# Optimization experiments

Hardware: AMD Instinct MI355X
Metric: run time of the kernel (lower is better)

The kernel has to match this reference:

```python
import jax, jax.numpy as jnp
import numpy as np
import math

B, S, T = 32, 128, 64
FEAT = 16
H = 1024
V = 32000


def _gru_step(x, h, wih, whh, bih, bhh):
    # torch nn.GRU cell: gates ordered (r, z, n)
    gi = x @ wih.T + bih
    gh = h @ whh.T + bhh
    ir, iz, in_ = jnp.split(gi, 3, axis=-1)
    hr, hz, hn = jnp.split(gh, 3, axis=-1)
    r = jax.nn.sigmoid(ir + hr)
    z = jax.nn.sigmoid(iz + hz)
    n = jnp.tanh(in_ + r * hn)
    return (1.0 - z) * n + z * h


def _forward(features, target_tokens, temp_W, temp_b, hum_W, hum_b, cloud_W, cloud_b,
             time_W, time_b, other_W, other_b, fi_W, fi_b,
             enc_wih, enc_whh, enc_bih, enc_bhh, emb, attn_W, attn_b,
             dec_wih, dec_whh, dec_bih, dec_bhh, out_W, out_b):
    b = features.shape[0]
    # per-feature projections (dropout = identity in eval mode)
    temp = features[:, :, 0:1] @ temp_W.T + temp_b
    hum = features[:, :, 1:2] @ hum_W.T + hum_b
    cloud = features[:, :, 2:3] @ cloud_W.T + cloud_b
    time = features[:, :, -5:-3] @ time_W.T + time_b
    other_in = jnp.concatenate([features[:, :, 3:-5], features[:, :, -3:]], axis=2)
    other = other_in @ other_W.T + other_b
    concat = jnp.concatenate([temp, hum, cloud, time, other], axis=2)  # [B,S,2H]
    proj = jnp.tanh(concat @ fi_W.T + fi_b)  # [B,S,H]

    # encoder GRU over time
    def enc_step(h, x):
        h2 = _gru_step(x, h, enc_wih, enc_whh, enc_bih, enc_bhh)
        return h2, h2
    h0 = jnp.zeros((b, H), proj.dtype)
    h_last, enc_outs = jax.lax.scan(enc_step, h0, proj.transpose(1, 0, 2))
    enc_out = enc_outs.transpose(1, 0, 2)  # [B,S,H]

    # attention keys computed once (loop-invariant in the original)
    keys = enc_out @ attn_W.T + attn_b  # [B,S,H]
    scale = 1.0 / math.sqrt(H)

    # decoder: teacher_forcing_ratio = 1.0 -> input at step t is target_tokens[:, t-1]
    def dec_step(h, tok):
        e = emb[tok]  # [B,H]
        scores = jnp.einsum('bh,bsh->bs', h, keys) * scale
        w = jax.nn.softmax(scores, axis=-1)
        ctx = jnp.einsum('bs,bsh->bh', w, enc_out)
        x = jnp.concatenate([e, ctx], axis=-1)  # [B,2H]
        h2 = _gru_step(x, h, dec_wih, dec_whh, dec_bih, dec_bhh)
        pred = jnp.concatenate([h2, ctx], axis=-1) @ out_W.T + out_b  # [B,V]
        return h2, pred

    _, preds = jax.lax.scan(dec_step, h_last, target_tokens[:, :-1].T)  # [T-1,B,V]
    outputs = jnp.zeros((b, target_tokens.shape[1], V), preds.dtype)
    outputs = outputs.at[:, 0, target_tokens[0, 0]].set(1.0)
    outputs = outputs.at[:, 1:, :].set(preds.transpose(1, 0, 2))
    return outputs


def setup_inputs() -> dict:
    key = jax.random.key(0)
    ks = jax.random.split(key, 32)
    nrm = lambda k, sh: jax.random.normal(k, sh, jnp.float32) * 0.05
    Hq = H // 4
    d = {}
    d['features'] = jax.random.normal(ks[0], (B, S, FEAT), jnp.float32)
    d['target_tokens'] = jax.random.randint(ks[1], (B, T), 0, V, dtype=jnp.int32)
    d['temp_W'] = nrm(ks[2], (Hq, 1)); d['temp_b'] = nrm(ks[3], (Hq,))
    d['hum_W'] = nrm(ks[4], (Hq, 1)); d['hum_b'] = nrm(ks[5], (Hq,))
    d['cloud_W'] = nrm(ks[6], (Hq, 1)); d['cloud_b'] = nrm(ks[7], (Hq,))
    d['time_W'] = nrm(ks[8], (Hq, 2)); d['time_b'] = nrm(ks[9], (Hq,))
    d['other_W'] = nrm(ks[10], (H, FEAT - 5)); d['other_b'] = nrm(ks[11], (H,))
    d['fi_W'] = nrm(ks[12], (H, 2 * H)); d['fi_b'] = nrm(ks[13], (H,))
    d['enc_wih'] = nrm(ks[14], (3 * H, H)); d['enc_whh'] = nrm(ks[15], (3 * H, H))
    d['enc_bih'] = nrm(ks[16], (3 * H,)); d['enc_bhh'] = nrm(ks[17], (3 * H,))
    d['emb'] = nrm(ks[18], (V, H))
    d['attn_W'] = nrm(ks[19], (H, H)); d['attn_b'] = nrm(ks[20], (H,))
    d['dec_wih'] = nrm(ks[21], (3 * H, 2 * H)); d['dec_whh'] = nrm(ks[22], (3 * H, H))
    d['dec_bih'] = nrm(ks[23], (3 * H,)); d['dec_bhh'] = nrm(ks[24], (3 * H,))
    d['out_W'] = nrm(ks[25], (V, 2 * H)); d['out_b'] = nrm(ks[26], (V,))
    return d


def reference(features, target_tokens, temp_W, temp_b, hum_W, hum_b, cloud_W, cloud_b,
              time_W, time_b, other_W, other_b, fi_W, fi_b,
              enc_wih, enc_whh, enc_bih, enc_bhh, emb, attn_W, attn_b,
              dec_wih, dec_whh, dec_bih, dec_bhh, out_W, out_b):
    return _forward(features, target_tokens, temp_W, temp_b, hum_W, hum_b, cloud_W, cloud_b,
                    time_W, time_b, other_W, other_b, fi_W, fi_b,
                    enc_wih, enc_whh, enc_bih, enc_bhh, emb, attn_W, attn_b,
                    dec_wih, dec_whh, dec_bih, dec_bhh, out_W, out_b)
```

## Files before the change

### kernel.cpp

```cpp
#include <hip/hip_runtime.h>

typedef float f32x4 __attribute__((ext_vector_type(4)));
typedef __bf16 bf16x8 __attribute__((ext_vector_type(8)));

#define DI static __device__ __forceinline__

DI unsigned short f2bf(float f) {
  unsigned u = __float_as_uint(f);
  u = (u + 0x7fffu + ((u >> 16) & 1u)) >> 16;
  return (unsigned short)u;
}
DI unsigned pk2(float lo, float hi) {
  return (unsigned)f2bf(lo) | ((unsigned)f2bf(hi) << 16);
}
DI float bflo(unsigned u) { return __uint_as_float(u << 16); }
DI float bfhi(unsigned u) { return __uint_as_float(u & 0xffff0000u); }
DI float sigm(float x) { return 1.0f / (1.0f + expf(-x)); }

DI void gl_lds16(const unsigned short* g, unsigned short* l) {
  __builtin_amdgcn_global_load_lds(
      (const __attribute__((address_space(1))) unsigned int*)g,
      (__attribute__((address_space(3))) unsigned int*)l, 16, 0, 0);
}

DI void st32_sc1(unsigned* p, unsigned v) {
  __hip_atomic_store(p, v, __ATOMIC_RELAXED, __HIP_MEMORY_SCOPE_AGENT);
}
DI void st64_sc1(unsigned long long* p, unsigned long long v) {
  __hip_atomic_store(p, v, __ATOMIC_RELAXED, __HIP_MEMORY_SCOPE_AGENT);
}
DI int ldw(const int* p) {
  return __hip_atomic_load(p, __ATOMIC_RELAXED, __HIP_MEMORY_SCOPE_AGENT);
}
DI void stw(int* p, int v) {
  __hip_atomic_store(p, v, __ATOMIC_RELAXED, __HIP_MEMORY_SCOPE_AGENT);
}

DI void waitrel(const int* relbase, int repl, int target) {
  const int* w = relbase + repl * 32;
  for (;;) {
    int v = 0;
    if ((threadIdx.x & 63) == 0) v = ldw(w);
    v = __shfl(v, 0);
    if (v >= target) break;
    __builtin_amdgcn_s_sleep(2);
  }
  asm volatile("" ::: "memory");
}
DI void strel(int* relbase, int v) {
  int l = threadIdx.x & 63;
  if (l < 8) stw(relbase + l * 32, v);
}

__global__ void k_fold(const float* __restrict__ tW, const float* __restrict__ tb,
                       const float* __restrict__ hW, const float* __restrict__ hb,
                       const float* __restrict__ cW, const float* __restrict__ cb,
                       const float* __restrict__ tiW, const float* __restrict__ tib,
                       const float* __restrict__ oW, const float* __restrict__ ob,
                       const float* __restrict__ fiW, const float* __restrict__ fib,
                       float* __restrict__ M, float* __restrict__ b0v)
{
  int g = blockIdx.x * 256 + threadIdx.x;
  if (g >= 1024 * 17) return;
  int h = g / 17, f = g - h * 17;
  const float* fw = fiW + (size_t)h * 2048;
  float s = 0.f;
  if (f == 16) {
    for (int k = 0; k < 256; ++k) s += fw[k] * tb[k];
    for (int k = 0; k < 256; ++k) s += fw[256 + k] * hb[k];
    for (int k = 0; k < 256; ++k) s += fw[512 + k] * cb[k];
    for (int k = 0; k < 256; ++k) s += fw[768 + k] * tib[k];
    for (int r = 0; r < 1024; ++r) s += fw[1024 + r] * ob[r];
    b0v[h] = s + fib[h];
  } else if (f == 0) {
    for (int k = 0; k < 256; ++k) s += fw[k] * tW[k];
    M[h * 16 + 0] = s;
  } else if (f == 1) {
    for (int k = 0; k < 256; ++k) s += fw[256 + k] * hW[k];
    M[h * 16 + 1] = s;
  } else if (f == 2) {
    for (int k = 0; k < 256; ++k) s += fw[512 + k] * cW[k];
    M[h * 16 + 2] = s;
  } else if (f == 11) {
    for (int k = 0; k < 256; ++k) s += fw[768 + k] * tiW[2 * k];
    M[h * 16 + 11] = s;
  } else if (f == 12) {
    for (int k = 0; k < 256; ++k) s += fw[768 + k] * tiW[2 * k + 1];
    M[h * 16 + 12] = s;
  } else {
    int col = (f <= 10) ? (f - 3) : (f - 5);
    for (int r = 0; r < 1024; ++r) s += fw[1024 + r] * oW[r * 11 + col];
    M[h * 16 + f] = s;
  }
}

__global__ __launch_bounds__(256)
void k_proj(const float* __restrict__ feat, const float* __restrict__ M,
            const float* __restrict__ b0v, unsigned short* __restrict__ proj)
{
  __shared__ float ft[16];
  int bs = blockIdx.x;
  int h = blockIdx.y * 256 + threadIdx.x;
  if (threadIdx.x < 16) ft[threadIdx.x] = feat[bs * 16 + threadIdx.x];
  __syncthreads();
  float sum = b0v[h];
  const float* mr = M + h * 16;
#pragma unroll
  for (int f = 0; f < 16; ++f) sum += mr[f] * ft[f];
  proj[(size_t)bs * 1024 + h] = f2bf(tanhf(sum));
}

__global__ void k_conv(const float* __restrict__ s, unsigned short* __restrict__ d, int n8)
{
  for (long i = (long)blockIdx.x * 256 + threadIdx.x; i < n8; i += (long)gridDim.x * 256) {
    const float* p = s + i * 8;
    f32x4 a = *(const f32x4*)p, b = *(const f32x4*)(p + 4);
    uint4 o;
    o.x = pk2(a[0], a[1]); o.y = pk2(a[2], a[3]);
    o.z = pk2(b[0], b[1]); o.w = pk2(b[2], b[3]);
    *(uint4*)(d + i * 8) = o;
  }
}

__global__ void k_conv_str(const float* __restrict__ s, unsigned short* __restrict__ d)
{
  int r = blockIdx.x;
  int c = threadIdx.x * 4;
  f32x4 a = *(const f32x4*)(s + (size_t)r * 2048 + c);
  uint2 o; o.x = pk2(a[0], a[1]); o.y = pk2(a[2], a[3]);
  *(uint2*)(d + (size_t)r * 1024 + c) = o;
}

__global__ void k_gather_e(const int* __restrict__ toks, const float* __restrict__ emb,
                           unsigned short* __restrict__ e_bf)
{
  int row = blockIdx.x;
  int t = row >> 5, b = row & 31;
  unsigned short* dst = e_bf + (size_t)row * 1024 + threadIdx.x * 4;
  if (t < 63) {
    int tok = toks[b * 64 + t];
    f32x4 a = *(const f32x4*)(emb + (size_t)tok * 1024 + threadIdx.x * 4);
    uint2 o; o.x = pk2(a[0], a[1]); o.y = pk2(a[2], a[3]);
    *(uint2*)dst = o;
  } else {
    uint2 o; o.x = 0u; o.y = 0u;
    *(uint2*)dst = o;
  }
}

__global__ void k_onehot(const int* __restrict__ toks, float* __restrict__ out)
{
  int i = blockIdx.x * 256 + threadIdx.x;
  if (i >= 32 * 32000) return;
  int b = i / 32000, v = i - b * 32000;
  out[(size_t)b * 64 * 32000 + v] = (v == toks[0]) ? 1.0f : 0.0f;
}

template<int MODE>
__global__ __launch_bounds__(256)
void gemm_bf(const unsigned short* __restrict__ A, const unsigned short* __restrict__ B,
             const float* __restrict__ bias, float* __restrict__ Cf,
             unsigned short* __restrict__ Cb,
             int tiles_m, int K, int lda, int ldb, int ldc, int coloff)
{
  __shared__ unsigned short As[4096];
  __shared__ unsigned short Bs[4096];
  const int nblk = gridDim.x;
  const int cpx = nblk >> 3;
  const int bid = blockIdx.x;
  const int id = (bid & 7) * cpx + (bid >> 3);
  const int tm = id % tiles_m, tn = id / tiles_m;
  const int tid = threadIdx.x;
  const int lane = tid & 63, wave = tid >> 6;
  const int wm = (wave & 1) << 6, wn = (wave >> 1) << 6;
  const int r0 = tid >> 2, kc0 = (tid & 3) << 3;
  const unsigned short* ga0 = A + (size_t)(tm * 128 + r0) * lda + kc0;
  const unsigned short* ga1 = A + (size_t)(tm * 128 + 64 + r0) * lda + kc0;
  const unsigned short* gb0 = B + (size_t)(tn * 128 + r0) * ldb + kc0;
  const unsigned short* gb1 = B + (size_t)(tn * 128 + 64 + r0) * ldb + kc0;
  const int lr = lane & 15, lkb = (lane >> 4) << 3;

  f32x4 acc[4][4];
#pragma unroll
  for (int m = 0; m < 4; ++m)
#pragma unroll
    for (int n = 0; n < 4; ++n) { acc[m][n][0]=0.f; acc[m][n][1]=0.f; acc[m][n][2]=0.f; acc[m][n][3]=0.f; }

  for (int kt = 0; kt < K; kt += 32) {
    __syncthreads();
    gl_lds16(ga0 + kt, &As[tid * 8]);
    gl_lds16(ga1 + kt, &As[(tid + 256) * 8]);
    gl_lds16(gb0 + kt, &Bs[tid * 8]);
    gl_lds16(gb1 + kt, &Bs[(tid + 256) * 8]);
    __syncthreads();
    bf16x8 af[4], bfv[4];
#pragma unroll
    for (int m = 0; m < 4; ++m) af[m] = *(const bf16x8*)&As[(wm + m * 16 + lr) * 32 + lkb];
#pragma unroll
    for (int n = 0; n < 4; ++n) bfv[n] = *(const bf16x8*)&Bs[(wn + n * 16 + lr) * 32 + lkb];
#pragma unroll
    for (int m = 0; m < 4; ++m)
#pragma unroll
      for (int n = 0; n < 4; ++n)
        acc[m][n] = __builtin_amdgcn_mfma_f32_16x16x32_bf16(af[m], bfv[n], acc[m][n], 0, 0, 0);
  }

#pragma unroll
  for (int m = 0; m < 4; ++m) {
    int rb = tm * 128 + wm + m * 16 + ((lane >> 4) << 2);
#pragma unroll
    for (int n = 0; n < 4; ++n) {
      int c = tn * 128 + wn + n * 16 + lr;
      float bb = bias[c];
#pragma unroll
      for (int i = 0; i < 4; ++i) {
        float v = acc[m][n][i] + bb;
        int r = rb + i;
        if (MODE == 0) {
          Cf[(size_t)r * ldc + c] = v;
        } else if (MODE == 1) {
          Cb[(size_t)r * ldc + c] = f2bf(v);
        } else {
          if (r < 2016) {
            int t = r >> 5, b2 = r & 31;
            Cf[((size_t)b2 * 64 + t + 1) * 32000 + coloff + c] = v;
          }
        }
      }
    }
  }
}

__global__ __launch_bounds__(256, 1)
void k_enc_scan(const float* __restrict__ gi_all, const float* __restrict__ whh,
                const float* __restrict__ bhh, float* __restrict__ hfp,
                unsigned short* __restrict__ enc_bf,
                int* __restrict__ arrE, int* __restrict__ relE)
{
  const int tid = threadIdx.x;
  const int blk = blockIdx.x;
  if (blk == 64) {
    if (tid < 64) {
      for (int g = 1; g <= 128; ++g) {
        for (;;) {
          int v = ldw(&arrE[tid << 4]);
          if (__all(v >= g)) break;
          __builtin_amdgcn_s_sleep(1);
        }
        asm volatile("" ::: "memory");
        strel(relE, g);
      }
    }
    return;
  }

  __shared__ unsigned short W[48 * 1024];
  __shared__ float Cred[4 * 2 * 3 * 64 * 4];
  const int lane = tid & 63, wave = tid >> 6;
  const int j0 = blk * 16;
  const int repl = blk & 7;

  for (int i = tid; i < 48 * 128; i += 256) {
    int r = i >> 7, c = i & 127;
    int gr = ((r >> 4) << 10) + j0 + (r & 15);
    const float* src = whh + ((size_t)gr << 10) + (c << 3);
    f32x4 a = *(const f32x4*)src, b = *(const f32x4*)(src + 4);
    uint4 o;
    o.x = pk2(a[0], a[1]); o.y = pk2(a[2], a[3]);
    o.z = pk2(b[0], b[1]); o.w = pk2(b[2], b[3]);
    *(uint4*)&W[(r << 10) + ((c ^ (r & 7)) << 3)] = o;
  }
  __syncthreads();

  int cb[2], cj[2], clb[2], creg[2], cm[2];
  float bh0[2], bh1[2], bh2[2];
  float hp[2] = {0.f, 0.f};
#pragma unroll
  for (int cc = 0; cc < 2; ++cc) {
    int cell = tid + (cc << 8);
    cb[cc] = cell >> 4; cj[cc] = cell & 15;
    clb[cc] = ((cb[cc] & 15) >> 2) * 16;
    creg[cc] = cb[cc] & 3; cm[cc] = cb[cc] >> 4;
    bh0[cc] = bhh[j0 + cj[cc]];
    bh1[cc] = bhh[1024 + j0 + cj[cc]];
    bh2[cc] = bhh[2048 + j0 + cj[cc]];
  }

#pragma unroll 1
  for (int s = 0; s < 128; ++s) {
    float gp[2][3];
#pragma unroll
    for (int cc = 0; cc < 2; ++cc) {
      const float* gi = gi_all + ((size_t)cb[cc] * 128 + s) * 3072 + j0 + cj[cc];
      gp[cc][0] = gi[0]; gp[cc][1] = gi[1024]; gp[cc][2] = gi[2048];
    }

    f32x4 acc[2][3];
#pragma unroll
    for (int m = 0; m < 2; ++m)
#pragma unroll
      for (int n = 0; n < 3; ++n) { acc[m][n][0]=0.f; acc[m][n][1]=0.f; acc[m][n][2]=0.f; acc[m][n][3]=0.f; }

    if (s > 0) {
      waitrel(relE, repl, s);
      const unsigned short* hr = enc_bf + (size_t)(s - 1) * 1024;
      const int k0 = wave << 8;
      bf16x8 af[2][8];
#pragma unroll
      for (int kk = 0; kk < 8; ++kk) {
        int k = k0 + kk * 32 + ((lane >> 4) << 3);
        af[0][kk] = *(const bf16x8*)(hr + (size_t)(lane & 15) * 131072 + k);
        af[1][kk] = *(const bf16x8*)(hr + (size_t)(16 + (lane & 15)) * 131072 + k);
      }
#pragma unroll
      for (int kk = 0; kk < 8; ++kk) {
        int c = ((k0 + kk * 32) >> 3) + (lane >> 4);
#pragma unroll
        for (int n = 0; n < 3; ++n) {
          int wr = n * 16 + (lane & 15);
          bf16x8 bfr = *(const bf16x8*)&W[(wr << 10) + ((c ^ (wr & 7)) << 3)];
          acc[0][n] = __builtin_amdgcn_mfma_f32_16x16x32_bf16(af[0][kk], bfr, acc[0][n], 0, 0, 0);
          acc[1][n] = __builtin_amdgcn_mfma_f32_16x16x32_bf16(af[1][kk], bfr, acc[1][n], 0, 0, 0);
        }
      }
    }
#pragma unroll
    for (int m = 0; m < 2; ++m)
#pragma unroll
      for (int n = 0; n < 3; ++n)
        *(f32x4*)&Cred[((((wave * 2 + m) * 3 + n) * 64) + lane) << 2] = acc[m][n];
    __syncthreads();

    float h2v[2];
#pragma unroll
    for (int cc = 0; cc < 2; ++cc) {
      int lj = clb[cc] + cj[cc], reg = creg[cc], m = cm[cc];
      float Cr = 0.f, Cz = 0.f, Cn = 0.f;
#pragma unroll
      for (int w = 0; w < 4; ++w) {
        Cr += Cred[((((w * 2 + m) * 3 + 0) * 64 + lj) << 2) + reg];
        Cz += Cred[((((w * 2 + m) * 3 + 1) * 64 + lj) << 2) + reg];
        Cn += Cred[((((w * 2 + m) * 3 + 2) * 64 + lj) << 2) + reg];
      }
      float r = sigm(gp[cc][0] + Cr + bh0[cc]);
      float z = sigm(gp[cc][1] + Cz + bh1[cc]);
      float n = tanhf(gp[cc][2] + r * (Cn + bh2[cc]));
      float h2 = (1.f - z) * n + z * hp[cc];
      h2v[cc] = h2; hp[cc] = h2;
    }
    if (s == 127) {
      hfp[cb[0] * 1024 + j0 + cj[0]] = h2v[0];
      hfp[cb[1] * 1024 + j0 + cj[1]] = h2v[1];
    }
    unsigned short s0 = f2bf(h2v[0]), s1 = f2bf(h2v[1]);
    unsigned o0 = (unsigned)__shfl_xor((int)(unsigned)s0, 1);
    unsigned o1 = (unsigned)__shfl_xor((int)(unsigned)s1, 1);
    if ((tid & 1) == 0) {
      int j = cj[0];
      st32_sc1((unsigned*)&enc_bf[((size_t)cb[0] * 128 + s) * 1024 + j0 + j],
               (unsigned)s0 | (o0 << 16));
      st32_sc1((unsigned*)&enc_bf[((size_t)cb[1] * 128 + s) * 1024 + j0 + j],
               (unsigned)s1 | (o1 << 16));
    }
    __syncthreads();
    if (tid == 0) stw(&arrE[blk << 4], s + 1);
  }
}

__global__ __launch_bounds__(256, 1)
void k_dec_scan(const float* __restrict__ gi_e, const float* __restrict__ whh,
                const float* __restrict__ wih, const float* __restrict__ bhh,
                const unsigned short* __restrict__ keys,
                const unsigned short* __restrict__ enc_bf,
                unsigned short* __restrict__ hcat, const float* __restrict__ hfp0,
                int* __restrict__ arrC, int* __restrict__ arrH,
                int* __restrict__ relD)
{
  const int tid = threadIdx.x;
  const int blk = blockIdx.x;
  const int repl = blk & 7;

  if (blk == 160) {
    if (tid < 64) {
      for (int t = 0; t < 63; ++t) {
        for (;;) {
          int v = (tid < 32) ? ldw(&arrC[tid << 4]) : 0x7fffffff;
          if (__all(v >= t + 1)) break;
          __builtin_amdgcn_s_sleep(1);
        }
        asm volatile("" ::: "memory");
        strel(relD, 2 * t + 1);
        for (;;) {
          int v0 = ldw(&arrH[(tid * 2) << 4]);
          int v1 = ldw(&arrH[(tid * 2 + 1) << 4]);
          if (__all(v0 >= t + 1 && v1 >= t + 1)) break;
          __builtin_amdgcn_s_sleep(1);
        }
        asm volatile("" ::: "memory");
        strel(relD, 2 * t + 2);
      }
    }
    return;
  }

  if (blk < 32) {
    __shared__ unsigned short hsh[1024];
    __shared__ float sarr[128];
    __shared__ float earr[128];
    const int b = blk;
#pragma unroll 1
    for (int t = 0; t < 63; ++t) {
      if (t) waitrel(relD, repl, 2 * t);
      const unsigned short* hsrc = (t == 0)
          ? (enc_bf + (size_t)b * 131072 + (size_t)127 * 1024)
          : (hcat + ((size_t)(t - 1) * 32 + b) * 2048);
      *(uint2*)&hsh[tid * 4] = *(const uint2*)(hsrc + tid * 4);
      __syncthreads();
      {
        int sp = tid >> 1, kh = (tid & 1) << 9;
        const unsigned short* kr = keys + ((size_t)b * 128 + sp) * 1024 + kh;
        float a0 = 0.f, a1 = 0.f, a2 = 0.f, a3 = 0.f;
#pragma unroll 8
        for (int c = 0; c < 512; c += 8) {
          uint4 kv = *(const uint4*)(kr + c);
          uint4 hv = *(const uint4*)&hsh[kh + c];
          a0 += bflo(kv.x) * bflo(hv.x) + bfhi(kv.x) * bfhi(hv.x);
          a1 += bflo(kv.y) * bflo(hv.y) + bfhi(kv.y) * bfhi(hv.y);
          a2 += bflo(kv.z) * bflo(hv.z) + bfhi(kv.z) * bfhi(hv.z);
          a3 += bflo(kv.w) * bflo(hv.w) + bfhi(kv.w) * bfhi(hv.w);
        }
        float a = (a0 + a1) + (a2 + a3);
        a += __shfl_xor(a, 1);
        if ((tid & 1) == 0) sarr[sp] = a * 0.03125f;
      }
      __syncthreads();
      float m0 = -1e30f, m1 = -1e30f, m2 = -1e30f, m3 = -1e30f;
#pragma unroll 8
      for (int i2 = 0; i2 < 128; i2 += 4) {
        m0 = fmaxf(m0, sarr[i2]); m1 = fmaxf(m1, sarr[i2 + 1]);
        m2 = fmaxf(m2, sarr[i2 + 2]); m3 = fmaxf(m3, sarr[i2 + 3]);
      }
      float mx = fmaxf(fmaxf(m0, m1), fmaxf(m2, m3));
      if (tid < 128) earr[tid] = expf(sarr[tid] - mx);
      __syncthreads();
      float s0 = 0.f, s1 = 0.f, s2 = 0.f, s3 = 0.f;
#pragma unroll 8
      for (int i2 = 0; i2 < 128; i2 += 4) {
        s0 += earr[i2]; s1 += earr[i2 + 1]; s2 += earr[i2 + 2]; s3 += earr[i2 + 3];
      }
      float winv = 1.f / ((s0 + s1) + (s2 + s3));
      f32x4 cacc; cacc[0]=0.f; cacc[1]=0.f; cacc[2]=0.f; cacc[3]=0.f;
      const unsigned short* eb = enc_bf + ((size_t)b << 17) + tid * 4;
#pragma unroll 4
      for (int s2i = 0; s2i < 128; ++s2i) {
        float w = earr[s2i] * winv;
        uint2 ev = *(const uint2*)(eb + ((size_t)s2i << 10));
        cacc[0] += w * bflo(ev.x); cacc[1] += w * bfhi(ev.x);
        cacc[2] += w * bflo(ev.y); cacc[3] += w * bfhi(ev.y);
      }
      unsigned long long cw = (unsigned long long)pk2(cacc[0], cacc[1])
                            | ((unsigned long long)pk2(cacc[2], cacc[3]) << 32);
      st64_sc1((unsigned long long*)(hcat + ((size_t)t * 32 + b) * 2048 + 1024 + tid * 4), cw);
      __syncthreads();
      if (tid == 0) stw(&arrC[blk << 4], t + 1);
    }
    return;
  }

  __shared__ unsigned short Wh[32 * 1024];
  __shared__ unsigned short Wx[32 * 1024];
  __shared__ float Cred[4 * 2 * 2 * 64 * 4];
  const int lane = tid & 63, wave = tid >> 6;
  const int gblk = blk - 32;
  const int j0 = gblk * 8;

  for (int i = tid; i < 32 * 128; i += 256) {
    int r = i >> 7, c = i & 127;
    int off = (r << 10) + ((c ^ (r & 7)) << 3);
    uint4 oh, ox;
    oh.x = oh.y = oh.z = oh.w = 0u; ox = oh;
    if (r < 24) {
      int gr = ((r >> 3) << 10) + j0 + (r & 7);
      const float* sh = whh + ((size_t)gr << 10) + (c << 3);
      f32x4 a = *(const f32x4*)sh, b = *(const f32x4*)(sh + 4);
      oh.x = pk2(a[0], a[1]); oh.y = pk2(a[2], a[3]);
      oh.z = pk2(b[0], b[1]); oh.w = pk2(b[2], b[3]);
      const float* sx = wih + ((size_t)gr << 11) + 1024 + (c << 3);
      f32x4 e = *(const f32x4*)sx, f = *(const f32x4*)(sx + 4);
      ox.x = pk2(e[0], e[1]); ox.y = pk2(e[2], e[3]);
      ox.z = pk2(f[0], f[1]); ox.w = pk2(f[2], f[3]);
    }
    *(uint4*)&Wh[off] = oh;
    *(uint4*)&Wx[off] = ox;
  }
  __syncthreads();

  const int gb = tid >> 3, gj = tid & 7;
  const int glb = ((gb & 15) >> 2) * 16;
  const int greg = gb & 3, gm = gb >> 4;
  const float bh0 = bhh[j0 + gj];
  const float bh1 = bhh[1024 + j0 + gj];
  const float bh2 = bhh[2048 + j0 + gj];
  float hpv = hfp0[gb * 1024 + j0 + gj];

#pragma unroll 1
  for (int t = 0; t < 63; ++t) {
    const float* gie = gi_e + ((size_t)t * 32 + gb) * 3072 + j0 + gj;
    float g0 = gie[0], g1 = gie[1024], g2 = gie[2048];

    const int part = wave >> 1;
    const int kh2 = (wave & 1) << 9;
    const unsigned short* abase;
    size_t astr;
    const unsigned short* Wl;
    if (part == 0) {
      if (t) waitrel(relD, repl, 2 * t);
      if (t == 0) { abase = enc_bf + (size_t)127 * 1024; astr = 131072; }
      else { abase = hcat + (size_t)(t - 1) * 32 * 2048; astr = 2048; }
      Wl = Wh;
    } else {
      waitrel(relD, repl, 2 * t + 1);
      abase = hcat + (size_t)t * 32 * 2048 + 1024; astr = 2048;
      Wl = Wx;
    }
    f32x4 acc[2][2];
#pragma unroll
    for (int m = 0; m < 2; ++m)
#pragma unroll
      for (int n = 0; n < 2; ++n) { acc[m][n][0]=0.f; acc[m][n][1]=0.f; acc[m][n][2]=0.f; acc[m][n][3]=0.f; }
#pragma unroll
    for (int hh = 0; hh < 2; ++hh) {
      bf16x8 af[2][8];
#pragma unroll
      for (int kk = 0; kk < 8; ++kk) {
        int k = kh2 + hh * 256 + kk * 32 + ((lane >> 4) << 3);
        af[0][kk] = *(const bf16x8*)(abase + (size_t)(lane & 15) * astr + k);
        af[1][kk] = *(const bf16x8*)(abase + (size_t)(16 + (lane & 15)) * astr + k);
      }
#pragma unroll
      for (int kk = 0; kk < 8; ++kk) {
        int c = ((kh2 + hh * 256 + kk * 32) >> 3) + (lane >> 4);
#pragma unroll
        for (int n = 0; n < 2; ++n) {
          int wr = n * 16 + (lane & 15);
          bf16x8 bfr = *(const bf16x8*)&Wl[(wr << 10) + ((c ^ (wr & 7)) << 3)];
          acc[0][n] = __builtin_amdgcn_mfma_f32_16x16x32_bf16(af[0][kk], bfr, acc[0][n], 0, 0, 0);
          acc[1][n] = __builtin_amdgcn_mfma_f32_16x16x32_bf16(af[1][kk], bfr, acc[1][n], 0, 0, 0);
        }
      }
    }
#pragma unroll
    for (int m = 0; m < 2; ++m)
#pragma unroll
      for (int n = 0; n < 2; ++n)
        *(f32x4*)&Cred[((((wave * 2 + m) * 2 + n) * 64) + lane) << 2] = acc[m][n];
    __syncthreads();

    {
      float Chr = 0.f, Chz = 0.f, Chn = 0.f, Cxr = 0.f, Cxz = 0.f, Cxn = 0.f;
#pragma unroll
      for (int w = 0; w < 2; ++w) {
        Chr += Cred[((((w * 2 + gm) * 2 + 0) * 64 + glb + gj) << 2) + greg];
        Chz += Cred[((((w * 2 + gm) * 2 + 0) * 64 + glb + gj + 8) << 2) + greg];
        Chn += Cred[((((w * 2 + gm) * 2 + 1) * 64 + glb + gj) << 2) + greg];
        Cxr += Cred[(((((w + 2) * 2 + gm) * 2 + 0) * 64 + glb + gj) << 2) + greg];
        Cxz += Cred[(((((w + 2) * 2 + gm) * 2 + 0) * 64 + glb + gj + 8) << 2) + greg];
        Cxn += Cred[(((((w + 2) * 2 + gm) * 2 + 1) * 64 + glb + gj) << 2) + greg];
      }
      float r = sigm(g0 + Cxr + Chr + bh0);
      float z = sigm(g1 + Cxz + Chz + bh1);
      float n2 = tanhf(g2 + Cxn + r * (Chn + bh2));
      float h2 = (1.f - z) * n2 + z * hpv;
      hpv = h2;
      unsigned short sv = f2bf(h2);
      unsigned ov = (unsigned)__shfl_xor((int)(unsigned)sv, 1);
      if ((tid & 1) == 0) {
        unsigned pv = (unsigned)sv | (ov << 16);
        st32_sc1((unsigned*)&hcat[((size_t)t * 32 + gb) * 2048 + j0 + gj], pv);
      }
    }
    __syncthreads();
    if (tid == 0) stw(&arrH[gblk << 4], t + 1);
  }
}

extern "C" void kernel_launch(void* const* d_in, const int* in_sizes, int n_in,
                              void* d_out, int out_size, void* d_ws, size_t ws_size,
                              hipStream_t stream)
{
  const float* features = (const float*)d_in[0];
  const int*   toks     = (const int*)d_in[1];
  const float* temp_W = (const float*)d_in[2];  const float* temp_b = (const float*)d_in[3];
  const float* hum_W  = (const float*)d_in[4];  const float* hum_b  = (const float*)d_in[5];
  const float* cloud_W= (const float*)d_in[6];  const float* cloud_b= (const float*)d_in[7];
  const float* time_W = (const float*)d_in[8];  const float* time_b = (const float*)d_in[9];
  const float* other_W= (const float*)d_in[10]; const float* other_b= (const float*)d_in[11];
  const float* fi_W   = (const float*)d_in[12]; const float* fi_b   = (const float*)d_in[13];
  const float* enc_wih= (const float*)d_in[14]; const float* enc_whh= (const float*)d_in[15];
  const float* enc_bih= (const float*)d_in[16]; const float* enc_bhh= (const float*)d_in[17];
  const float* emb    = (const float*)d_in[18];
  const float* attn_W = (const float*)d_in[19]; const float* attn_b = (const float*)d_in[20];
  const float* dec_wih= (const float*)d_in[21]; const float* dec_whh= (const float*)d_in[22];
  const float* dec_bih= (const float*)d_in[23]; const float* dec_bhh= (const float*)d_in[24];
  const float* out_W  = (const float*)d_in[25]; const float* out_b  = (const float*)d_in[26];
  float* out = (float*)d_out;
  char* ws = (char*)d_ws;

  int*            arrE    = (int*)(ws + 0);
  int*            arrH    = (int*)(ws + 4096);
  int*            arrC    = (int*)(ws + 12288);
  int*            relE    = (int*)(ws + 14336);
  int*            relD    = (int*)(ws + 15360);
  float*          Mf      = (float*)(ws + 16384);
  float*          b0v     = (float*)(ws + 81920);
  float*          hfp     = (float*)(ws + 86016);
  unsigned short* hcat    = (unsigned short*)(ws + 217088);
  unsigned short* keys_bf = (unsigned short*)(ws + 8605696);
  unsigned short* enc_bf  = (unsigned short*)(ws + 16994304);
  float*          gi_e    = (float*)(ws + 25382912);
  float*          gi_all  = (float*)(ws + 50548736);
  unsigned short* proj_bf = (unsigned short*)(ws + 100880384);
  unsigned short* e_bf    = (unsigned short*)(ws + 109268992);
  unsigned short* wihE_bf = (unsigned short*)(ws + 113463296);
  unsigned short* attnW_bf= (unsigned short*)(ws + 119754752);
  unsigned short* wihD_bf = (unsigned short*)(ws + 121851904);
  unsigned short* outW_bf = (unsigned short*)(ws + 25382912);

  hipMemsetAsync(ws, 0, 16384, stream);
  hipMemsetAsync(ws + 217088 + (size_t)2016 * 2048 * 2, 0, 32 * 2048 * 2, stream);

  k_conv<<<1536, 256, 0, stream>>>(enc_wih, wihE_bf, 393216);
  k_conv<<<512, 256, 0, stream>>>(attn_W, attnW_bf, 131072);
  k_conv_str<<<3072, 256, 0, stream>>>(dec_wih, wihD_bf);

  k_fold<<<68, 256, 0, stream>>>(temp_W, temp_b, hum_W, hum_b, cloud_W, cloud_b,
                                 time_W, time_b, other_W, other_b, fi_W, fi_b, Mf, b0v);
  k_proj<<<dim3(4096, 4), 256, 0, stream>>>(features, Mf, b0v, proj_bf);

  gemm_bf<0><<<768, 256, 0, stream>>>(proj_bf, wihE_bf, enc_bih, gi_all, nullptr,
                                      32, 1024, 1024, 1024, 3072, 0);
  k_enc_scan<<<65, 256, 0, stream>>>(gi_all, enc_whh, enc_bhh, hfp, enc_bf, arrE, relE);

  gemm_bf<1><<<256, 256, 0, stream>>>(enc_bf, attnW_bf, attn_b, nullptr, keys_bf,
                                      32, 1024, 1024, 1024, 1024, 0);
  k_gather_e<<<2048, 256, 0, stream>>>(toks, emb, e_bf);
  gemm_bf<0><<<384, 256, 0, stream>>>(e_bf, wihD_bf, dec_bih, gi_e, nullptr,
                                      16, 1024, 1024, 1024, 3072, 0);
  k_dec_scan<<<161, 256, 0, stream>>>(gi_e, dec_whh, dec_wih, dec_bhh, keys_bf,
                                      enc_bf, hcat, hfp, arrC, arrH, relD);

  k_conv<<<2048, 256, 0, stream>>>(out_W, outW_bf, 4096000);
  gemm_bf<2><<<2000, 256, 0, stream>>>(hcat, outW_bf, out_b, out, nullptr,
                                       16, 2048, 2048, 2048, 0, 0);
  k_conv<<<2048, 256, 0, stream>>>(out_W + (size_t)16000 * 2048, outW_bf, 4096000);
  gemm_bf<2><<<2000, 256, 0, stream>>>(hcat, outW_bf, out_b + 16000, out, nullptr,
                                       16, 2048, 2048, 2048, 0, 16000);
  k_onehot<<<4000, 256, 0, stream>>>(toks, out);
}
```

Before: 2.645 ms.

## Precompute encoder-projected context weights to shorten decoder recurrence critical path

Rewrites the decoder's context-to-gate input as attention weights times a precomputed (enc_out @ Wih_ctx) tensor produced by an extra GEMM before the scan. The attention blocks now publish softmax weights instead of the context vector, so gate blocks no longer wait on the context MFMA pass and the barrier per step drops from two phases to one. Spin waits switch from s_sleep to a short FMA burn loop, and hidden-state stores widen to 64-bit. This adds a large upfront GEMM, an extra transposed weight conversion and a strided dot product per gate element, and it changes rounding order.

```diff
diff --git a/kernel.cpp b/kernel.cpp
--- a/kernel.cpp
+++ b/kernel.cpp
@@ -34,6 +34,13 @@
 }
 DI void stw(int* p, int v) {
   __hip_atomic_store(p, v, __ATOMIC_RELAXED, __HIP_MEMORY_SCOPE_AGENT);
+}
+
+DI void burn(int n) {
+  float x = (float)(int)threadIdx.x;
+#pragma unroll 1
+  for (int i = 0; i < n; ++i) x = __builtin_fmaf(x, 1.0000001f, 1e-9f);
+  asm volatile("" :: "v"(x));
 }
 
 DI void waitrel(const int* relbase, int repl, int target) {
@@ -43,13 +50,23 @@
     if ((threadIdx.x & 63) == 0) v = ldw(w);
     v = __shfl(v, 0);
     if (v >= target) break;
-    __builtin_amdgcn_s_sleep(2);
+    burn(60);
   }
   asm volatile("" ::: "memory");
 }
 DI void strel(int* relbase, int v) {
   int l = threadIdx.x & 63;
   if (l < 8) stw(relbase + l * 32, v);
+}
+DI void wait_arr32(const int* arr, int target) {
+  const int l = (int)(threadIdx.x & 63);
+  const int* p = arr + (l << 3);
+  for (;;) {
+    int v = (l < 32) ? ldw(p) : target;
+    if (__all(v >= target)) break;
+    burn(60);
+  }
+  asm volatile("" ::: "memory");
 }
 
 __global__ void k_fold(const float* __restrict__ tW, const float* __restrict__ tb,
@@ -122,11 +139,11 @@
   }
 }
 
-__global__ void k_conv_str(const float* __restrict__ s, unsigned short* __restrict__ d)
+__global__ void k_conv_str(const float* __restrict__ s, unsigned short* __restrict__ d, int coff)
 {
   int r = blockIdx.x;
   int c = threadIdx.x * 4;
-  f32x4 a = *(const f32x4*)(s + (size_t)r * 2048 + c);
+  f32x4 a = *(const f32x4*)(s + (size_t)r * 2048 + coff + c);
   uint2 o; o.x = pk2(a[0], a[1]); o.y = pk2(a[2], a[3]);
   *(uint2*)(d + (size_t)r * 1024 + c) = o;
 }
@@ -220,6 +237,8 @@
           Cf[(size_t)r * ldc + c] = v;
         } else if (MODE == 1) {
           Cb[(size_t)r * ldc + c] = f2bf(v);
+        } else if (MODE == 3) {
+          Cb[(size_t)c * 4096 + r] = f2bf(v);
         } else {
           if (r < 2016) {
             int t = r >> 5, b2 = r & 31;
@@ -241,11 +260,11 @@
   const int blk = blockIdx.x;
   if (blk == 64) {
     if (tid < 64) {
-      for (int g = 1; g <= 128; ++g) {
+      for (int g = 1; g <= 127; ++g) {
         for (;;) {
-          int v = ldw(&arrE[tid << 4]);
+          int v = ldw(&arrE[tid << 3]);
           if (__all(v >= g)) break;
-          __builtin_amdgcn_s_sleep(1);
+          burn(60);
         }
         asm volatile("" ::: "memory");
         strel(relE, g);
@@ -352,29 +371,30 @@
       hfp[cb[0] * 1024 + j0 + cj[0]] = h2v[0];
       hfp[cb[1] * 1024 + j0 + cj[1]] = h2v[1];
     }
-    unsigned short s0 = f2bf(h2v[0]), s1 = f2bf(h2v[1]);
-    unsigned o0 = (unsigned)__shfl_xor((int)(unsigned)s0, 1);
-    unsigned o1 = (unsigned)__shfl_xor((int)(unsigned)s1, 1);
-    if ((tid & 1) == 0) {
-      int j = cj[0];
-      st32_sc1((unsigned*)&enc_bf[((size_t)cb[0] * 128 + s) * 1024 + j0 + j],
-               (unsigned)s0 | (o0 << 16));
-      st32_sc1((unsigned*)&enc_bf[((size_t)cb[1] * 128 + s) * 1024 + j0 + j],
-               (unsigned)s1 | (o1 << 16));
+#pragma unroll
+    for (int cc = 0; cc < 2; ++cc) {
+      unsigned short sv = f2bf(h2v[cc]);
+      unsigned p = (unsigned)sv | (((unsigned)__shfl_xor((int)(unsigned)sv, 1)) << 16);
+      unsigned q = (unsigned)__shfl_xor((int)p, 2);
+      if ((tid & 3) == 0) {
+        unsigned long long dv = (unsigned long long)p | ((unsigned long long)q << 32);
+        st64_sc1((unsigned long long*)&enc_bf[((size_t)cb[cc] * 128 + s) * 1024 + j0 + cj[cc]], dv);
+      }
     }
     __syncthreads();
-    if (tid == 0) stw(&arrE[blk << 4], s + 1);
+    if (tid == 0) stw(&arrE[blk << 3], s + 1);
   }
 }
 
 __global__ __launch_bounds__(256, 1)
 void k_dec_scan(const float* __restrict__ gi_e, const float* __restrict__ whh,
-                const float* __restrict__ wih, const float* __restrict__ bhh,
+                const float* __restrict__ bhh,
                 const unsigned short* __restrict__ keys,
                 const unsigned short* __restrict__ enc_bf,
                 unsigned short* __restrict__ hcat, const float* __restrict__ hfp0,
-                int* __restrict__ arrC, int* __restrict__ arrH,
-                int* __restrict__ relD)
+                const unsigned short* __restrict__ xeT, float* __restrict__ w_all,
+                int* __restrict__ arrW, int* __restrict__ arrH,
+                int* __restrict__ relH)
 {
   const int tid = threadIdx.x;
   const int blk = blockIdx.x;
@@ -382,22 +402,15 @@
 
   if (blk == 160) {
     if (tid < 64) {
-      for (int t = 0; t < 63; ++t) {
-        for (;;) {
-          int v = (tid < 32) ? ldw(&arrC[tid << 4]) : 0x7fffffff;
-          if (__all(v >= t + 1)) break;
-          __builtin_amdgcn_s_sleep(1);
-        }
-        asm volatile("" ::: "memory");
-        strel(relD, 2 * t + 1);
+      for (int g = 1; g <= 62; ++g) {
         for (;;) {
           int v0 = ldw(&arrH[(tid * 2) << 4]);
           int v1 = ldw(&arrH[(tid * 2 + 1) << 4]);
-          if (__all(v0 >= t + 1 && v1 >= t + 1)) break;
-          __builtin_amdgcn_s_sleep(1);
+          if (__all(v0 >= g && v1 >= g)) break;
+          burn(60);
         }
         asm volatile("" ::: "memory");
-        strel(relD, 2 * t + 2);
+        strel(relH, g);
       }
     }
     return;
@@ -410,7 +423,7 @@
     const int b = blk;
 #pragma unroll 1
     for (int t = 0; t < 63; ++t) {
-      if (t) waitrel(relD, repl, 2 * t);
+      if (t) waitrel(relH, repl, t);
       const unsigned short* hsrc = (t == 0)
           ? (enc_bf + (size_t)b * 131072 + (size_t)127 * 1024)
           : (hcat + ((size_t)(t - 1) * 32 + b) * 2048);
@@ -449,6 +462,14 @@
         s0 += earr[i2]; s1 += earr[i2 + 1]; s2 += earr[i2 + 2]; s3 += earr[i2 + 3];
       }
       float winv = 1.f / ((s0 + s1) + (s2 + s3));
+      if (tid < 64) {
+        unsigned lo = __float_as_uint(earr[tid * 2] * winv);
+        unsigned hi = __float_as_uint(earr[tid * 2 + 1] * winv);
+        st64_sc1((unsigned long long*)(w_all + ((size_t)t * 32 + b) * 128 + tid * 2),
+                 (unsigned long long)lo | ((unsigned long long)hi << 32));
+      }
+      __syncthreads();
+      if (tid == 0) stw(&arrW[b << 3], t + 1);
       f32x4 cacc; cacc[0]=0.f; cacc[1]=0.f; cacc[2]=0.f; cacc[3]=0.f;
       const unsigned short* eb = enc_bf + ((size_t)b << 17) + tid * 4;
 #pragma unroll 4
@@ -458,17 +479,13 @@
         cacc[0] += w * bflo(ev.x); cacc[1] += w * bfhi(ev.x);
         cacc[2] += w * bflo(ev.y); cacc[3] += w * bfhi(ev.y);
       }
-      unsigned long long cw = (unsigned long long)pk2(cacc[0], cacc[1])
-                            | ((unsigned long long)pk2(cacc[2], cacc[3]) << 32);
-      st64_sc1((unsigned long long*)(hcat + ((size_t)t * 32 + b) * 2048 + 1024 + tid * 4), cw);
-      __syncthreads();
-      if (tid == 0) stw(&arrC[blk << 4], t + 1);
+      uint2 co; co.x = pk2(cacc[0], cacc[1]); co.y = pk2(cacc[2], cacc[3]);
+      *(uint2*)(hcat + ((size_t)t * 32 + b) * 2048 + 1024 + tid * 4) = co;
     }
     return;
   }
 
   __shared__ unsigned short Wh[32 * 1024];
-  __shared__ unsigned short Wx[32 * 1024];
   __shared__ float Cred[4 * 2 * 2 * 64 * 4];
   const int lane = tid & 63, wave = tid >> 6;
   const int gblk = blk - 32;
@@ -477,21 +494,16 @@
   for (int i = tid; i < 32 * 128; i += 256) {
     int r = i >> 7, c = i & 127;
     int off = (r << 10) + ((c ^ (r & 7)) << 3);
-    uint4 oh, ox;
-    oh.x = oh.y = oh.z = oh.w = 0u; ox = oh;
+    uint4 oh;
+    oh.x = oh.y = oh.z = oh.w = 0u;
     if (r < 24) {
       int gr = ((r >> 3) << 10) + j0 + (r & 7);
       const float* sh = whh + ((size_t)gr << 10) + (c << 3);
       f32x4 a = *(const f32x4*)sh, b = *(const f32x4*)(sh + 4);
       oh.x = pk2(a[0], a[1]); oh.y = pk2(a[2], a[3]);
       oh.z = pk2(b[0], b[1]); oh.w = pk2(b[2], b[3]);
-      const float* sx = wih + ((size_t)gr << 11) + 1024 + (c << 3);
-      f32x4 e = *(const f32x4*)sx, f = *(const f32x4*)(sx + 4);
-      ox.x = pk2(e[0], e[1]); ox.y = pk2(e[2], e[3]);
-      ox.z = pk2(f[0], f[1]); ox.w = pk2(f[2], f[3]);
     }
     *(uint4*)&Wh[off] = oh;
-    *(uint4*)&Wx[off] = ox;
   }
   __syncthreads();
 
@@ -502,48 +514,41 @@
   const float bh1 = bhh[1024 + j0 + gj];
   const float bh2 = bhh[2048 + j0 + gj];
   float hpv = hfp0[gb * 1024 + j0 + gj];
+  const unsigned short* x0 = xeT + ((size_t)(j0 + gj) << 12) + gb * 128;
+  const unsigned short* x1 = xeT + ((size_t)(1024 + j0 + gj) << 12) + gb * 128;
+  const unsigned short* x2 = xeT + ((size_t)(2048 + j0 + gj) << 12) + gb * 128;
 
 #pragma unroll 1
   for (int t = 0; t < 63; ++t) {
     const float* gie = gi_e + ((size_t)t * 32 + gb) * 3072 + j0 + gj;
     float g0 = gie[0], g1 = gie[1024], g2 = gie[2048];
 
-    const int part = wave >> 1;
-    const int kh2 = (wave & 1) << 9;
+    if (t) waitrel(relH, repl, t);
     const unsigned short* abase;
     size_t astr;
-    const unsigned short* Wl;
-    if (part == 0) {
-      if (t) waitrel(relD, repl, 2 * t);
-      if (t == 0) { abase = enc_bf + (size_t)127 * 1024; astr = 131072; }
-      else { abase = hcat + (size_t)(t - 1) * 32 * 2048; astr = 2048; }
-      Wl = Wh;
-    } else {
-      waitrel(relD, repl, 2 * t + 1);
-      abase = hcat + (size_t)t * 32 * 2048 + 1024; astr = 2048;
-      Wl = Wx;
-    }
+    if (t == 0) { abase = enc_bf + (size_t)127 * 1024; astr = 131072; }
+    else { abase = hcat + (size_t)(t - 1) * 32 * 2048; astr = 2048; }
+    const int k0 = wave << 8;
     f32x4 acc[2][2];
 #pragma unroll
     for (int m = 0; m < 2; ++m)
 #pragma unroll
       for (int n = 0; n < 2; ++n) { acc[m][n][0]=0.f; acc[m][n][1]=0.f; acc[m][n][2]=0.f; acc[m][n][3]=0.f; }
-#pragma unroll
-    for (int hh = 0; hh < 2; ++hh) {
+    {
       bf16x8 af[2][8];
 #pragma unroll
       for (int kk = 0; kk < 8; ++kk) {
-        int k = kh2 + hh * 256 + kk * 32 + ((lane >> 4) << 3);
+        int k = k0 + kk * 32 + ((lane >> 4) << 3);
         af[0][kk] = *(const bf16x8*)(abase + (size_t)(lane & 15) * astr + k);
         af[1][kk] = *(const bf16x8*)(abase + (size_t)(16 + (lane & 15)) * astr + k);
       }
 #pragma unroll
       for (int kk = 0; kk < 8; ++kk) {
-        int c = ((kh2 + hh * 256 + kk * 32) >> 3) + (lane >> 4);
+        int c = ((k0 + kk * 32) >> 3) + (lane >> 4);
 #pragma unroll
         for (int n = 0; n < 2; ++n) {
           int wr = n * 16 + (lane & 15);
-          bf16x8 bfr = *(const bf16x8*)&Wl[(wr << 10) + ((c ^ (wr & 7)) << 3)];
+          bf16x8 bfr = *(const bf16x8*)&Wh[(wr << 10) + ((c ^ (wr & 7)) << 3)];
           acc[0][n] = __builtin_amdgcn_mfma_f32_16x16x32_bf16(af[0][kk], bfr, acc[0][n], 0, 0, 0);
           acc[1][n] = __builtin_amdgcn_mfma_f32_16x16x32_bf16(af[1][kk], bfr, acc[1][n], 0, 0, 0);
         }
@@ -556,27 +561,43 @@
         *(f32x4*)&Cred[((((wave * 2 + m) * 2 + n) * 64) + lane) << 2] = acc[m][n];
     __syncthreads();
 
+    wait_arr32(arrW, t + 1);
+    float cx0 = 0.f, cx1 = 0.f, cx2 = 0.f;
+    const float* wrow = w_all + ((size_t)t * 32 + gb) * 128;
+#pragma unroll 4
+    for (int s = 0; s < 128; s += 8) {
+      f32x4 wa = *(const f32x4*)(wrow + s);
+      f32x4 wb2 = *(const f32x4*)(wrow + s + 4);
+      uint4 a0 = *(const uint4*)(x0 + s);
+      uint4 a1 = *(const uint4*)(x1 + s);
+      uint4 a2 = *(const uint4*)(x2 + s);
+      cx0 += wa[0]*bflo(a0.x) + wa[1]*bfhi(a0.x) + wa[2]*bflo(a0.y) + wa[3]*bfhi(a0.y)
+           + wb2[0]*bflo(a0.z) + wb2[1]*bfhi(a0.z) + wb2[2]*bflo(a0.w) + wb2[3]*bfhi(a0.w);
+      cx1 += wa[0]*bflo(a1.x) + wa[1]*bfhi(a1.x) + wa[2]*bflo(a1.y) + wa[3]*bfhi(a1.y)
+           + wb2[0]*bflo(a1.z) + wb2[1]*bfhi(a1.z) + wb2[2]*bflo(a1.w) + wb2[3]*bfhi(a1.w);
+      cx2 += wa[0]*bflo(a2.x) + wa[1]*bfhi(a2.x) + wa[2]*bflo(a2.y) + wa[3]*bfhi(a2.y)
+           + wb2[0]*bflo(a2.z) + wb2[1]*bfhi(a2.z) + wb2[2]*bflo(a2.w) + wb2[3]*bfhi(a2.w);
+    }
+
     {
-      float Chr = 0.f, Chz = 0.f, Chn = 0.f, Cxr = 0.f, Cxz = 0.f, Cxn = 0.f;
-#pragma unroll
-      for (int w = 0; w < 2; ++w) {
+      float Chr = 0.f, Chz = 0.f, Chn = 0.f;
+#pragma unroll
+      for (int w = 0; w < 4; ++w) {
         Chr += Cred[((((w * 2 + gm) * 2 + 0) * 64 + glb + gj) << 2) + greg];
         Chz += Cred[((((w * 2 + gm) * 2 + 0) * 64 + glb + gj + 8) << 2) + greg];
         Chn += Cred[((((w * 2 + gm) * 2 + 1) * 64 + glb + gj) << 2) + greg];
-        Cxr += Cred[(((((w + 2) * 2 + gm) * 2 + 0) * 64 + glb + gj) << 2) + greg];
-        Cxz += Cred[(((((w + 2) * 2 + gm) * 2 + 0) * 64 + glb + gj + 8) << 2) + greg];
-        Cxn += Cred[(((((w + 2) * 2 + gm) * 2 + 1) * 64 + glb + gj) << 2) + greg];
-      }
-      float r = sigm(g0 + Cxr + Chr + bh0);
-      float z = sigm(g1 + Cxz + Chz + bh1);
-      float n2 = tanhf(g2 + Cxn + r * (Chn + bh2));
+      }
+      float r = sigm(g0 + cx0 + Chr + bh0);
+      float z = sigm(g1 + cx1 + Chz + bh1);
+      float n2 = tanhf(g2 + cx2 + r * (Chn + bh2));
       float h2 = (1.f - z) * n2 + z * hpv;
       hpv = h2;
       unsigned short sv = f2bf(h2);
-      unsigned ov = (unsigned)__shfl_xor((int)(unsigned)sv, 1);
-      if ((tid & 1) == 0) {
-        unsigned pv = (unsigned)sv | (ov << 16);
-        st32_sc1((unsigned*)&hcat[((size_t)t * 32 + gb) * 2048 + j0 + gj], pv);
+      unsigned p = (unsigned)sv | (((unsigned)__shfl_xor((int)(unsigned)sv, 1)) << 16);
+      unsigned q = (unsigned)__shfl_xor((int)p, 2);
+      if ((tid & 3) == 0) {
+        unsigned long long dv = (unsigned long long)p | ((unsigned long long)q << 32);
+        st64_sc1((unsigned long long*)&hcat[((size_t)t * 32 + gb) * 2048 + j0 + gj], dv);
       }
     }
     __syncthreads();
@@ -608,30 +629,35 @@
 
   int*            arrE    = (int*)(ws + 0);
   int*            arrH    = (int*)(ws + 4096);
-  int*            arrC    = (int*)(ws + 12288);
+  int*            arrW    = (int*)(ws + 12288);
   int*            relE    = (int*)(ws + 14336);
-  int*            relD    = (int*)(ws + 15360);
-  float*          Mf      = (float*)(ws + 16384);
-  float*          b0v     = (float*)(ws + 81920);
-  float*          hfp     = (float*)(ws + 86016);
-  unsigned short* hcat    = (unsigned short*)(ws + 217088);
-  unsigned short* keys_bf = (unsigned short*)(ws + 8605696);
-  unsigned short* enc_bf  = (unsigned short*)(ws + 16994304);
-  float*          gi_e    = (float*)(ws + 25382912);
-  float*          gi_all  = (float*)(ws + 50548736);
-  unsigned short* proj_bf = (unsigned short*)(ws + 100880384);
-  unsigned short* e_bf    = (unsigned short*)(ws + 109268992);
-  unsigned short* wihE_bf = (unsigned short*)(ws + 113463296);
-  unsigned short* attnW_bf= (unsigned short*)(ws + 119754752);
-  unsigned short* wihD_bf = (unsigned short*)(ws + 121851904);
-  unsigned short* outW_bf = (unsigned short*)(ws + 25382912);
-
-  hipMemsetAsync(ws, 0, 16384, stream);
-  hipMemsetAsync(ws + 217088 + (size_t)2016 * 2048 * 2, 0, 32 * 2048 * 2, stream);
+  int*            relH    = (int*)(ws + 15360);
+  float*          zbias   = (float*)(ws + 16384);
+  float*          Mf      = (float*)(ws + 32768);
+  float*          b0v     = (float*)(ws + 98304);
+  float*          hfp     = (float*)(ws + 102400);
+  unsigned short* hcat    = (unsigned short*)(ws + 233472);
+  unsigned short* keys_bf = (unsigned short*)(ws + 8622080);
+  unsigned short* enc_bf  = (unsigned short*)(ws + 17010688);
+  float*          w_all   = (float*)(ws + 25399296);
+  float*          gi_e    = (float*)(ws + 26447872);
+  unsigned short* xeT     = (unsigned short*)(ws + 51613696);
+  float*          gi_all  = (float*)(ws + 76779520);
+  unsigned short* proj_bf = (unsigned short*)(ws + 127111168);
+  unsigned short* e_bf    = (unsigned short*)(ws + 135499776);
+  unsigned short* wihE_bf = (unsigned short*)(ws + 139694080);
+  unsigned short* attnW_bf= (unsigned short*)(ws + 145985536);
+  unsigned short* wihD_bf = (unsigned short*)(ws + 148082688);
+  unsigned short* wihDc_bf= (unsigned short*)(ws + 154374144);
+  unsigned short* outW_bf = (unsigned short*)(ws + 26447872);
+
+  hipMemsetAsync(ws, 0, 32768, stream);
+  hipMemsetAsync(ws + 233472 + (size_t)2016 * 2048 * 2, 0, 32 * 2048 * 2, stream);
 
   k_conv<<<1536, 256, 0, stream>>>(enc_wih, wihE_bf, 393216);
   k_conv<<<512, 256, 0, stream>>>(attn_W, attnW_bf, 131072);
-  k_conv_str<<<3072, 256, 0, stream>>>(dec_wih, wihD_bf);
+  k_conv_str<<<3072, 256, 0, stream>>>(dec_wih, wihD_bf, 0);
+  k_conv_str<<<3072, 256, 0, stream>>>(dec_wih, wihDc_bf, 1024);
 
   k_fold<<<68, 256, 0, stream>>>(temp_W, temp_b, hum_W, hum_b, cloud_W, cloud_b,
                                  time_W, time_b, other_W, other_b, fi_W, fi_b, Mf, b0v);
@@ -646,8 +672,10 @@
   k_gather_e<<<2048, 256, 0, stream>>>(toks, emb, e_bf);
   gemm_bf<0><<<384, 256, 0, stream>>>(e_bf, wihD_bf, dec_bih, gi_e, nullptr,
                                       16, 1024, 1024, 1024, 3072, 0);
-  k_dec_scan<<<161, 256, 0, stream>>>(gi_e, dec_whh, dec_wih, dec_bhh, keys_bf,
-                                      enc_bf, hcat, hfp, arrC, arrH, relD);
+  gemm_bf<3><<<768, 256, 0, stream>>>(enc_bf, wihDc_bf, zbias, nullptr, xeT,
+                                      32, 1024, 1024, 1024, 0, 0);
+  k_dec_scan<<<161, 256, 0, stream>>>(gi_e, dec_whh, dec_bhh, keys_bf, enc_bf,
+                                      hcat, hfp, xeT, w_all, arrW, arrH, relH);
 
   k_conv<<<2048, 256, 0, stream>>>(out_W, outW_bf, 4096000);
   gemm_bf<2><<<2000, 256, 0, stream>>>(hcat, outW_bf, out_b, out, nullptr,
```

Result: slower. 2.910 ms (+10.0%).
